# Performance work log

Hardware: AMD Instinct MI355X
Metric: run time of the kernel (lower is better)

## Reference

```python
import jax, jax.numpy as jnp
import numpy as np

B = 8192            # batch.size
NNZ = B * 32        # active features per position ~32
FT = 512            # ft_out
F_FULL = 49152      # HalfKA feature count
F_VIRT = 768        # factorized (virtual) feature count


def setup_inputs() -> dict:
    key = jax.random.key(0)
    ks = jax.random.split(key, 8)
    s_ft = 1.0 / np.sqrt(F_FULL).astype(np.float32)
    s_fft = 1.0 / np.sqrt(F_VIRT).astype(np.float32)
    s_out = 1.0 / np.sqrt(2 * FT).astype(np.float32)
    return {
        "values": jnp.ones((NNZ,), dtype=jnp.float32),
        # W_ft stored feature-major [F_FULL, FT] = torch ft.weight.T, so rows are gathered per feature
        "W_ft": jax.random.uniform(ks[0], (F_FULL, FT), jnp.float32, -s_ft, s_ft),
        "ft_b": jax.random.uniform(ks[1], (FT,), jnp.float32, -s_ft, s_ft),
        "W_fft": jax.random.uniform(ks[2], (F_VIRT, FT), jnp.float32, -s_fft, s_fft),
        "fft_b": jax.random.uniform(ks[3], (FT,), jnp.float32, -s_fft, s_fft),
        "W_out": jax.random.uniform(ks[4], (1, 2 * FT), jnp.float32, -s_out, s_out),
        "out_b": jax.random.uniform(ks[5], (1,), jnp.float32, -s_out, s_out),
        "batch_ids": jnp.sort(jax.random.randint(ks[6], (NNZ,), 0, B)),
        "stm_feat": jax.random.randint(ks[7], (NNZ,), 0, F_FULL),
        "nstm_feat": jax.random.randint(jax.random.fold_in(key, 7), (NNZ,), 0, F_FULL),
        "size": B,
    }


def reference(values, W_ft, ft_b, W_fft, fft_b, W_out, out_b,
              batch_ids, stm_feat, nstm_feat, size):
    v = values[:, None]  # [NNZ, 1]

    def transform(feat):
        # sparse COO x dense weight == gather weight rows per active feature, scale, segment-sum
        acc = jax.ops.segment_sum(W_ft[feat] * v, batch_ids, num_segments=size)
        acc_v = jax.ops.segment_sum(W_fft[feat % F_VIRT] * v, batch_ids, num_segments=size)
        return acc + acc_v + ft_b + fft_b  # both Linear biases applied once per row

    stm_ft = transform(stm_feat)    # [B, FT]
    nstm_ft = transform(nstm_feat)  # [B, FT]
    hidden = jnp.clip(jnp.concatenate([stm_ft, nstm_ft], axis=1), 0.0, 1.0)
    return jax.nn.sigmoid(hidden @ W_out.T + out_b)  # [B, 1]
```

## Files before the change

### kernel.cpp

```cpp
#include <hip/hip_runtime.h>
#include <hip/hip_bf16.h>
#include <math.h>


constexpr int FT      = 512;
constexpr int FV      = 768;
constexpr int CHUNK   = 64;

typedef __attribute__((ext_vector_type(8))) unsigned short ushort8_t;

__device__ inline unsigned short f2bf(float x) {
    union { float f; unsigned int u; } v; v.f = x;
    unsigned int r = v.u + 0x7FFFu + ((v.u >> 16) & 1u);
    return (unsigned short)(r >> 16);
}
__device__ inline float bf2f(unsigned short s) {
    union { unsigned int u; float f; } v; v.u = ((unsigned int)s) << 16;
    return v.f;
}

__global__ __launch_bounds__(256)
void bounds_kernel(const int* __restrict__ batch_ids, int nnz, int B,
                   int* __restrict__ seg_start)
{
    int b = blockIdx.x * 256 + threadIdx.x;
    if (b > B) return;
    int lo = 0, hi = nnz;
    while (lo < hi) {
        int mid = (lo + hi) >> 1;
        if (batch_ids[mid] < b) lo = mid + 1; else hi = mid;
    }
    seg_start[b] = lo;
}

__global__ __launch_bounds__(256)
void convert_kernel(const float* __restrict__ W_ft, const float* __restrict__ W_fft,
                    unsigned short* __restrict__ comb, int n8)
{
    int i = blockIdx.x * 256 + threadIdx.x;
    if (i >= n8) return;
    const int f    = i >> 6;
    const int gcol = (i & 63) * 8;
    const int base = i * 8;
    const int vrow = (f % FV) * FT + gcol;

    const float4 a0 = *(const float4*)(W_ft  + base);
    const float4 a1 = *(const float4*)(W_ft  + base + 4);
    const float4 b0 = *(const float4*)(W_fft + vrow);
    const float4 b1 = *(const float4*)(W_fft + vrow + 4);

    ushort8_t u;
    u[0] = f2bf(a0.x + b0.x); u[1] = f2bf(a0.y + b0.y);
    u[2] = f2bf(a0.z + b0.z); u[3] = f2bf(a0.w + b0.w);
    u[4] = f2bf(a1.x + b1.x); u[5] = f2bf(a1.y + b1.y);
    u[6] = f2bf(a1.z + b1.z); u[7] = f2bf(a1.w + b1.w);
    *(ushort8_t*)(comb + base) = u;
}

__global__ __launch_bounds__(256)
void nnue4_kernel(const float* __restrict__ values,
                  const unsigned short* __restrict__ Wc,
                  const float* __restrict__ ft_b,
                  const float* __restrict__ fft_b,
                  const float* __restrict__ W_out,
                  const float* __restrict__ out_b,
                  const int*   __restrict__ seg_start,
                  const int*   __restrict__ stm_feat,
                  const int*   __restrict__ nstm_feat,
                  float* __restrict__ out)
{
    const int b    = blockIdx.x;
    const int t    = threadIdx.x;
    const int wid  = t >> 6;
    const int lane = t & 63;
    const int col  = lane * 8;

    const int seg_lo = seg_start[b];
    const int seg_hi = seg_start[b + 1];

    __shared__ int   sh_os[CHUNK];
    __shared__ int   sh_on[CHUNK];
    __shared__ float sh_v [CHUNK];
    __shared__ float sh_part[3][2][FT];

    float acc_s[8] = {0,0,0,0,0,0,0,0};
    float acc_n[8] = {0,0,0,0,0,0,0,0};

    for (int base = seg_lo; base < seg_hi; base += CHUNK) {
        const int cnt = min(CHUNK, seg_hi - base);
        __syncthreads();
        if (t < cnt) {
            sh_os[t] = stm_feat [base + t] * FT;
            sh_on[t] = nstm_feat[base + t] * FT;
            sh_v [t] = values[base + t];
        }
        __syncthreads();

        #pragma unroll 4
        for (int j = wid; j < cnt; j += 4) {
            const float v = sh_v[j];
            const ushort8_t a = *(const ushort8_t*)(Wc + sh_os[j] + col);
            const ushort8_t c = *(const ushort8_t*)(Wc + sh_on[j] + col);
            #pragma unroll
            for (int k = 0; k < 8; ++k) {
                acc_s[k] = fmaf(bf2f(a[k]), v, acc_s[k]);
                acc_n[k] = fmaf(bf2f(c[k]), v, acc_n[k]);
            }
        }
    }

    __syncthreads();
    if (wid > 0) {
        #pragma unroll
        for (int k = 0; k < 8; ++k) {
            sh_part[wid - 1][0][col + k] = acc_s[k];
            sh_part[wid - 1][1][col + k] = acc_n[k];
        }
    }
    __syncthreads();

    if (wid == 0) {
        #pragma unroll
        for (int k = 0; k < 8; ++k) {
            acc_s[k] += sh_part[0][0][col + k] + sh_part[1][0][col + k] + sh_part[2][0][col + k];
            acc_n[k] += sh_part[0][1][col + k] + sh_part[1][1][col + k] + sh_part[2][1][col + k];
        }

        const float4 fb0 = *(const float4*)(ft_b  + col);
        const float4 fb1 = *(const float4*)(ft_b  + col + 4);
        const float4 vb0 = *(const float4*)(fft_b + col);
        const float4 vb1 = *(const float4*)(fft_b + col + 4);
        const float4 ws0 = *(const float4*)(W_out + col);
        const float4 ws1 = *(const float4*)(W_out + col + 4);
        const float4 wn0 = *(const float4*)(W_out + FT + col);
        const float4 wn1 = *(const float4*)(W_out + FT + col + 4);

        const float bias[8] = { fb0.x + vb0.x, fb0.y + vb0.y, fb0.z + vb0.z, fb0.w + vb0.w,
                                fb1.x + vb1.x, fb1.y + vb1.y, fb1.z + vb1.z, fb1.w + vb1.w };
        const float wos[8]  = { ws0.x, ws0.y, ws0.z, ws0.w, ws1.x, ws1.y, ws1.z, ws1.w };
        const float won[8]  = { wn0.x, wn0.y, wn0.z, wn0.w, wn1.x, wn1.y, wn1.z, wn1.w };

        float partial = 0.f;
        #pragma unroll
        for (int k = 0; k < 8; ++k) {
            float hs = fminf(fmaxf(acc_s[k] + bias[k], 0.f), 1.f);
            float hn = fminf(fmaxf(acc_n[k] + bias[k], 0.f), 1.f);
            partial = fmaf(hs, wos[k], partial);
            partial = fmaf(hn, won[k], partial);
        }

        #pragma unroll
        for (int off = 32; off > 0; off >>= 1)
            partial += __shfl_down(partial, off, 64);

        if (lane == 0)
            out[b] = 1.0f / (1.0f + expf(-(partial + out_b[0])));
    }
}

__global__ __launch_bounds__(128)
void nnue_f32_kernel(const float* __restrict__ values,
                     const float* __restrict__ W_ft,
                     const float* __restrict__ ft_b,
                     const float* __restrict__ W_fft,
                     const float* __restrict__ fft_b,
                     const float* __restrict__ W_out,
                     const float* __restrict__ out_b,
                     const int*   __restrict__ batch_ids,
                     const int*   __restrict__ stm_feat,
                     const int*   __restrict__ nstm_feat,
                     int nnz,
                     float* __restrict__ out)
{
    const int b   = blockIdx.x;
    const int t   = threadIdx.x;
    const int col = t * 4;

    int lo0 = 0, hi0 = nnz;
    while (lo0 < hi0) {
        int mid = (lo0 + hi0) >> 1;
        if (batch_ids[mid] < b) lo0 = mid + 1; else hi0 = mid;
    }
    int lo1 = lo0, hi1 = nnz;
    while (lo1 < hi1) {
        int mid = (lo1 + hi1) >> 1;
        if (batch_ids[mid] < b + 1) lo1 = mid + 1; else hi1 = mid;
    }
    const int seg_lo = lo0, seg_hi = lo1;

    __shared__ int   sh_off_s [128];
    __shared__ int   sh_off_sv[128];
    __shared__ int   sh_off_n [128];
    __shared__ int   sh_off_nv[128];
    __shared__ float sh_v     [128];

    float4 acc_s = make_float4(0.f, 0.f, 0.f, 0.f);
    float4 acc_n = make_float4(0.f, 0.f, 0.f, 0.f);

    for (int base = seg_lo; base < seg_hi; base += 128) {
        const int cnt = min(128, seg_hi - base);
        __syncthreads();
        if (t < cnt) {
            int fs = stm_feat[base + t];
            int fn = nstm_feat[base + t];
            sh_off_s [t] = fs * FT;
            sh_off_sv[t] = (fs % FV) * FT;
            sh_off_n [t] = fn * FT;
            sh_off_nv[t] = (fn % FV) * FT;
            sh_v     [t] = values[base + t];
        }
        __syncthreads();

        #pragma unroll 2
        for (int j = 0; j < cnt; ++j) {
            const float v = sh_v[j];
            const float4 a  = *(const float4*)(W_ft  + sh_off_s [j] + col);
            const float4 av = *(const float4*)(W_fft + sh_off_sv[j] + col);
            const float4 c  = *(const float4*)(W_ft  + sh_off_n [j] + col);
            const float4 cv = *(const float4*)(W_fft + sh_off_nv[j] + col);
            acc_s.x = fmaf(a.x + av.x, v, acc_s.x);
            acc_s.y = fmaf(a.y + av.y, v, acc_s.y);
            acc_s.z = fmaf(a.z + av.z, v, acc_s.z);
            acc_s.w = fmaf(a.w + av.w, v, acc_s.w);
            acc_n.x = fmaf(c.x + cv.x, v, acc_n.x);
            acc_n.y = fmaf(c.y + cv.y, v, acc_n.y);
            acc_n.z = fmaf(c.z + cv.z, v, acc_n.z);
            acc_n.w = fmaf(c.w + cv.w, v, acc_n.w);
        }
    }

    const float4 fb  = *(const float4*)(ft_b  + col);
    const float4 vb  = *(const float4*)(fft_b + col);
    const float4 wos = *(const float4*)(W_out + col);
    const float4 won = *(const float4*)(W_out + FT + col);

    float partial = 0.f;
    {
        float h;
        h = fminf(fmaxf(acc_s.x + fb.x + vb.x, 0.f), 1.f); partial = fmaf(h, wos.x, partial);
        h = fminf(fmaxf(acc_s.y + fb.y + vb.y, 0.f), 1.f); partial = fmaf(h, wos.y, partial);
        h = fminf(fmaxf(acc_s.z + fb.z + vb.z, 0.f), 1.f); partial = fmaf(h, wos.z, partial);
        h = fminf(fmaxf(acc_s.w + fb.w + vb.w, 0.f), 1.f); partial = fmaf(h, wos.w, partial);
        h = fminf(fmaxf(acc_n.x + fb.x + vb.x, 0.f), 1.f); partial = fmaf(h, won.x, partial);
        h = fminf(fmaxf(acc_n.y + fb.y + vb.y, 0.f), 1.f); partial = fmaf(h, won.y, partial);
        h = fminf(fmaxf(acc_n.z + fb.z + vb.z, 0.f), 1.f); partial = fmaf(h, won.z, partial);
        h = fminf(fmaxf(acc_n.w + fb.w + vb.w, 0.f), 1.f); partial = fmaf(h, won.w, partial);
    }

    #pragma unroll
    for (int off = 32; off > 0; off >>= 1)
        partial += __shfl_down(partial, off, 64);

    __shared__ float wave_sum[2];
    if ((t & 63) == 0) wave_sum[t >> 6] = partial;
    __syncthreads();
    if (t == 0) {
        float s = wave_sum[0] + wave_sum[1] + out_b[0];
        out[b] = 1.0f / (1.0f + expf(-s));
    }
}

extern "C" void kernel_launch(void* const* d_in, const int* in_sizes, int n_in,
                              void* d_out, int out_size, void* d_ws, size_t ws_size,
                              hipStream_t stream) {
    const float* values    = (const float*)d_in[0];
    const float* W_ft      = (const float*)d_in[1];
    const float* ft_b      = (const float*)d_in[2];
    const float* W_fft     = (const float*)d_in[3];
    const float* fft_b     = (const float*)d_in[4];
    const float* W_out     = (const float*)d_in[5];
    const float* out_b     = (const float*)d_in[6];
    const int*   batch_ids = (const int*)d_in[7];
    const int*   stm_feat  = (const int*)d_in[8];
    const int*   nstm_feat = (const int*)d_in[9];

    const int nnz  = in_sizes[0];
    const int B    = out_size;
    const int n_ft = in_sizes[1];

    const size_t comb_bytes = (size_t)n_ft * sizeof(unsigned short);
    const size_t need = comb_bytes + (size_t)(B + 1) * sizeof(int);

    if (ws_size >= need) {
        unsigned short* comb = (unsigned short*)d_ws;
        int* seg_start = (int*)((char*)d_ws + comb_bytes);

        const int n8    = n_ft / 8;
        const int cgrid = (n8 + 255) / 256;
        const int bgrid = (B + 1 + 255) / 256;

        bounds_kernel<<<bgrid, 256, 0, stream>>>(batch_ids, nnz, B, seg_start);
        convert_kernel<<<cgrid, 256, 0, stream>>>(W_ft, W_fft, comb, n8);
        nnue4_kernel<<<B, 256, 0, stream>>>(
            values, comb, ft_b, fft_b, W_out, out_b,
            seg_start, stm_feat, nstm_feat, (float*)d_out);
    } else {
        nnue_f32_kernel<<<B, 128, 0, stream>>>(
            values, W_ft, ft_b, W_fft, fft_b, W_out, out_b,
            batch_ids, stm_feat, nstm_feat, nnz, (float*)d_out);
    }
}
```

Baseline: 221.8 us.

## Merge prepass kernels and process four rows per two-wave block

Fuses the segment-bounds search and the bf16 weight-combine conversion into one prepass launch, which removes a kernel launch. The main kernel now uses 128 threads (two wavefronts), and each block handles four batch rows in sequence with a larger index chunk, so the cross-wave reduction is smaller. The cost is fewer wavefronts in flight per row, which may hide less gather latency, and a fallback path taken when B is not a multiple of four.

New measurement: 215.6 us. 1.03x faster.

```diff
diff --git a/kernel.cpp b/kernel.cpp
--- a/kernel.cpp
+++ b/kernel.cpp
@@ -5,7 +5,8 @@
 
 constexpr int FT      = 512;
 constexpr int FV      = 768;
-constexpr int CHUNK   = 64;
+constexpr int CHUNK   = 128;
+constexpr int ROWS    = 4;
 
 typedef __attribute__((ext_vector_type(8))) unsigned short ushort8_t;
 
@@ -20,141 +21,142 @@
 }
 
 __global__ __launch_bounds__(256)
-void bounds_kernel(const int* __restrict__ batch_ids, int nnz, int B,
-                   int* __restrict__ seg_start)
+void prepass_kernel(const float* __restrict__ W_ft, const float* __restrict__ W_fft,
+                    unsigned short* __restrict__ comb, int n8, int cgrid,
+                    const int* __restrict__ batch_ids, int nnz, int B,
+                    int* __restrict__ seg_start)
 {
-    int b = blockIdx.x * 256 + threadIdx.x;
-    if (b > B) return;
-    int lo = 0, hi = nnz;
-    while (lo < hi) {
-        int mid = (lo + hi) >> 1;
-        if (batch_ids[mid] < b) lo = mid + 1; else hi = mid;
-    }
-    seg_start[b] = lo;
-}
-
-__global__ __launch_bounds__(256)
-void convert_kernel(const float* __restrict__ W_ft, const float* __restrict__ W_fft,
-                    unsigned short* __restrict__ comb, int n8)
+    if (blockIdx.x < (unsigned)cgrid) {
+        int i = blockIdx.x * 256 + threadIdx.x;
+        if (i >= n8) return;
+        const int f    = i >> 6;
+        const int base = i * 8;
+        const int gcol = (i & 63) * 8;
+        const int vrow = (f % FV) * FT + gcol;
+
+        const float4 a0 = *(const float4*)(W_ft  + base);
+        const float4 a1 = *(const float4*)(W_ft  + base + 4);
+        const float4 b0 = *(const float4*)(W_fft + vrow);
+        const float4 b1 = *(const float4*)(W_fft + vrow + 4);
+
+        ushort8_t u;
+        u[0] = f2bf(a0.x + b0.x); u[1] = f2bf(a0.y + b0.y);
+        u[2] = f2bf(a0.z + b0.z); u[3] = f2bf(a0.w + b0.w);
+        u[4] = f2bf(a1.x + b1.x); u[5] = f2bf(a1.y + b1.y);
+        u[6] = f2bf(a1.z + b1.z); u[7] = f2bf(a1.w + b1.w);
+        *(ushort8_t*)(comb + base) = u;
+    } else {
+        int b = (blockIdx.x - cgrid) * 256 + threadIdx.x;
+        if (b > B) return;
+        int lo = 0, hi = nnz;
+        while (lo < hi) {
+            int mid = (lo + hi) >> 1;
+            if (batch_ids[mid] < b) lo = mid + 1; else hi = mid;
+        }
+        seg_start[b] = lo;
+    }
+}
+
+__global__ __launch_bounds__(128)
+void nnue_kernel(const float* __restrict__ values,
+                 const unsigned short* __restrict__ Wc,
+                 const float* __restrict__ ft_b,
+                 const float* __restrict__ fft_b,
+                 const float* __restrict__ W_out,
+                 const float* __restrict__ out_b,
+                 const int*   __restrict__ seg_start,
+                 const int*   __restrict__ stm_feat,
+                 const int*   __restrict__ nstm_feat,
+                 float* __restrict__ out)
 {
-    int i = blockIdx.x * 256 + threadIdx.x;
-    if (i >= n8) return;
-    const int f    = i >> 6;
-    const int gcol = (i & 63) * 8;
-    const int base = i * 8;
-    const int vrow = (f % FV) * FT + gcol;
-
-    const float4 a0 = *(const float4*)(W_ft  + base);
-    const float4 a1 = *(const float4*)(W_ft  + base + 4);
-    const float4 b0 = *(const float4*)(W_fft + vrow);
-    const float4 b1 = *(const float4*)(W_fft + vrow + 4);
-
-    ushort8_t u;
-    u[0] = f2bf(a0.x + b0.x); u[1] = f2bf(a0.y + b0.y);
-    u[2] = f2bf(a0.z + b0.z); u[3] = f2bf(a0.w + b0.w);
-    u[4] = f2bf(a1.x + b1.x); u[5] = f2bf(a1.y + b1.y);
-    u[6] = f2bf(a1.z + b1.z); u[7] = f2bf(a1.w + b1.w);
-    *(ushort8_t*)(comb + base) = u;
-}
-
-__global__ __launch_bounds__(256)
-void nnue4_kernel(const float* __restrict__ values,
-                  const unsigned short* __restrict__ Wc,
-                  const float* __restrict__ ft_b,
-                  const float* __restrict__ fft_b,
-                  const float* __restrict__ W_out,
-                  const float* __restrict__ out_b,
-                  const int*   __restrict__ seg_start,
-                  const int*   __restrict__ stm_feat,
-                  const int*   __restrict__ nstm_feat,
-                  float* __restrict__ out)
-{
-    const int b    = blockIdx.x;
     const int t    = threadIdx.x;
-    const int wid  = t >> 6;
+    const int w    = t >> 6;
     const int lane = t & 63;
     const int col  = lane * 8;
-
-    const int seg_lo = seg_start[b];
-    const int seg_hi = seg_start[b + 1];
 
     __shared__ int   sh_os[CHUNK];
     __shared__ int   sh_on[CHUNK];
     __shared__ float sh_v [CHUNK];
-    __shared__ float sh_part[3][2][FT];
-
-    float acc_s[8] = {0,0,0,0,0,0,0,0};
-    float acc_n[8] = {0,0,0,0,0,0,0,0};
-
-    for (int base = seg_lo; base < seg_hi; base += CHUNK) {
-        const int cnt = min(CHUNK, seg_hi - base);
+    __shared__ float sh_part[2][FT];
+
+    for (int r = 0; r < ROWS; ++r) {
+        const int b      = blockIdx.x * ROWS + r;
+        const int seg_lo = seg_start[b];
+        const int seg_hi = seg_start[b + 1];
+
+        float acc_s[8] = {0,0,0,0,0,0,0,0};
+        float acc_n[8] = {0,0,0,0,0,0,0,0};
+
+        for (int base = seg_lo; base < seg_hi; base += CHUNK) {
+            const int cnt = min(CHUNK, seg_hi - base);
+            __syncthreads();
+            if (t < cnt) {
+                sh_os[t] = stm_feat [base + t] * FT;
+                sh_on[t] = nstm_feat[base + t] * FT;
+                sh_v [t] = values[base + t];
+            }
+            __syncthreads();
+
+            #pragma unroll 4
+            for (int j = w; j < cnt; j += 2) {
+                const float v = sh_v[j];
+                const ushort8_t a = *(const ushort8_t*)(Wc + sh_os[j] + col);
+                const ushort8_t c = *(const ushort8_t*)(Wc + sh_on[j] + col);
+                #pragma unroll
+                for (int k = 0; k < 8; ++k) {
+                    acc_s[k] = fmaf(bf2f(a[k]), v, acc_s[k]);
+                    acc_n[k] = fmaf(bf2f(c[k]), v, acc_n[k]);
+                }
+            }
+        }
+
         __syncthreads();
-        if (t < cnt) {
-            sh_os[t] = stm_feat [base + t] * FT;
-            sh_on[t] = nstm_feat[base + t] * FT;
-            sh_v [t] = values[base + t];
-        }
-        __syncthreads();
-
-        #pragma unroll 4
-        for (int j = wid; j < cnt; j += 4) {
-            const float v = sh_v[j];
-            const ushort8_t a = *(const ushort8_t*)(Wc + sh_os[j] + col);
-            const ushort8_t c = *(const ushort8_t*)(Wc + sh_on[j] + col);
+        if (w == 1) {
             #pragma unroll
             for (int k = 0; k < 8; ++k) {
-                acc_s[k] = fmaf(bf2f(a[k]), v, acc_s[k]);
-                acc_n[k] = fmaf(bf2f(c[k]), v, acc_n[k]);
-            }
-        }
-    }
-
-    __syncthreads();
-    if (wid > 0) {
-        #pragma unroll
-        for (int k = 0; k < 8; ++k) {
-            sh_part[wid - 1][0][col + k] = acc_s[k];
-            sh_part[wid - 1][1][col + k] = acc_n[k];
-        }
-    }
-    __syncthreads();
-
-    if (wid == 0) {
-        #pragma unroll
-        for (int k = 0; k < 8; ++k) {
-            acc_s[k] += sh_part[0][0][col + k] + sh_part[1][0][col + k] + sh_part[2][0][col + k];
-            acc_n[k] += sh_part[0][1][col + k] + sh_part[1][1][col + k] + sh_part[2][1][col + k];
-        }
-
-        const float4 fb0 = *(const float4*)(ft_b  + col);
-        const float4 fb1 = *(const float4*)(ft_b  + col + 4);
-        const float4 vb0 = *(const float4*)(fft_b + col);
-        const float4 vb1 = *(const float4*)(fft_b + col + 4);
-        const float4 ws0 = *(const float4*)(W_out + col);
-        const float4 ws1 = *(const float4*)(W_out + col + 4);
-        const float4 wn0 = *(const float4*)(W_out + FT + col);
-        const float4 wn1 = *(const float4*)(W_out + FT + col + 4);
-
-        const float bias[8] = { fb0.x + vb0.x, fb0.y + vb0.y, fb0.z + vb0.z, fb0.w + vb0.w,
-                                fb1.x + vb1.x, fb1.y + vb1.y, fb1.z + vb1.z, fb1.w + vb1.w };
-        const float wos[8]  = { ws0.x, ws0.y, ws0.z, ws0.w, ws1.x, ws1.y, ws1.z, ws1.w };
-        const float won[8]  = { wn0.x, wn0.y, wn0.z, wn0.w, wn1.x, wn1.y, wn1.z, wn1.w };
-
-        float partial = 0.f;
-        #pragma unroll
-        for (int k = 0; k < 8; ++k) {
-            float hs = fminf(fmaxf(acc_s[k] + bias[k], 0.f), 1.f);
-            float hn = fminf(fmaxf(acc_n[k] + bias[k], 0.f), 1.f);
-            partial = fmaf(hs, wos[k], partial);
-            partial = fmaf(hn, won[k], partial);
-        }
-
-        #pragma unroll
-        for (int off = 32; off > 0; off >>= 1)
-            partial += __shfl_down(partial, off, 64);
-
-        if (lane == 0)
-            out[b] = 1.0f / (1.0f + expf(-(partial + out_b[0])));
+                sh_part[0][col + k] = acc_s[k];
+                sh_part[1][col + k] = acc_n[k];
+            }
+        }
+        __syncthreads();
+
+        if (w == 0) {
+            #pragma unroll
+            for (int k = 0; k < 8; ++k) {
+                acc_s[k] += sh_part[0][col + k];
+                acc_n[k] += sh_part[1][col + k];
+            }
+
+            const float4 fb0 = *(const float4*)(ft_b  + col);
+            const float4 fb1 = *(const float4*)(ft_b  + col + 4);
+            const float4 vb0 = *(const float4*)(fft_b + col);
+            const float4 vb1 = *(const float4*)(fft_b + col + 4);
+            const float4 ws0 = *(const float4*)(W_out + col);
+            const float4 ws1 = *(const float4*)(W_out + col + 4);
+            const float4 wn0 = *(const float4*)(W_out + FT + col);
+            const float4 wn1 = *(const float4*)(W_out + FT + col + 4);
+
+            const float bias[8] = { fb0.x + vb0.x, fb0.y + vb0.y, fb0.z + vb0.z, fb0.w + vb0.w,
+                                    fb1.x + vb1.x, fb1.y + vb1.y, fb1.z + vb1.z, fb1.w + vb1.w };
+            const float wos[8]  = { ws0.x, ws0.y, ws0.z, ws0.w, ws1.x, ws1.y, ws1.z, ws1.w };
+            const float won[8]  = { wn0.x, wn0.y, wn0.z, wn0.w, wn1.x, wn1.y, wn1.z, wn1.w };
+
+            float partial = 0.f;
+            #pragma unroll
+            for (int k = 0; k < 8; ++k) {
+                float hs = fminf(fmaxf(acc_s[k] + bias[k], 0.f), 1.f);
+                float hn = fminf(fmaxf(acc_n[k] + bias[k], 0.f), 1.f);
+                partial = fmaf(hs, wos[k], partial);
+                partial = fmaf(hn, won[k], partial);
+            }
+
+            #pragma unroll
+            for (int off = 32; off > 0; off >>= 1)
+                partial += __shfl_down(partial, off, 64);
+
+            if (lane == 0)
+                out[b] = 1.0f / (1.0f + expf(-(partial + out_b[0])));
+        }
     }
 }
 
@@ -281,7 +283,7 @@
     const size_t comb_bytes = (size_t)n_ft * sizeof(unsigned short);
     const size_t need = comb_bytes + (size_t)(B + 1) * sizeof(int);
 
-    if (ws_size >= need) {
+    if (ws_size >= need && (B % ROWS) == 0) {
         unsigned short* comb = (unsigned short*)d_ws;
         int* seg_start = (int*)((char*)d_ws + comb_bytes);
 
@@ -289,9 +291,9 @@
         const int cgrid = (n8 + 255) / 256;
         const int bgrid = (B + 1 + 255) / 256;
 
-        bounds_kernel<<<bgrid, 256, 0, stream>>>(batch_ids, nnz, B, seg_start);
-        convert_kernel<<<cgrid, 256, 0, stream>>>(W_ft, W_fft, comb, n8);
-        nnue4_kernel<<<B, 256, 0, stream>>>(
+        prepass_kernel<<<cgrid + bgrid, 256, 0, stream>>>(
+            W_ft, W_fft, comb, n8, cgrid, batch_ids, nnz, B, seg_start);
+        nnue_kernel<<<B / ROWS, 128, 0, stream>>>(
             values, comb, ft_b, fft_b, W_out, out_b,
             seg_start, stm_feat, nstm_feat, (float*)d_out);
     } else {
```
